# Optimization experiments

Measured on AMD Instinct MI355X. Metric: run time of the kernel, lower is better.

The kernel has to match this reference:

```python
import jax, jax.numpy as jnp
import numpy as np

N = 200000      # num nodes
E = 3200000     # num LBO edges (avg degree 16)
FIN = 64
FOUT = 64
K = 6           # Chebyshev order


def setup_inputs() -> dict:
    key = jax.random.key(0)
    k0, k1, k2, k3 = jax.random.split(key, 4)
    x = jax.random.normal(k0, (N, FIN), dtype=jnp.float32)
    LBO_index = jax.random.randint(k1, (2, E), 0, N)
    LBO_weight = jax.random.normal(k2, (E,), dtype=jnp.float32)
    stdv = float(np.sqrt(6.0 / (FIN + FOUT)))  # glorot uniform
    weight = jax.random.uniform(k3, (K, FIN, FOUT), dtype=jnp.float32,
                                minval=-stdv, maxval=stdv)
    bias = jnp.zeros((FOUT,), dtype=jnp.float32)
    return {"x": x, "LBO_index": LBO_index, "LBO_weight": LBO_weight,
            "weight": weight, "bias": bias}


def reference(x, LBO_index, LBO_weight, weight, bias):
    # __norm__: scale Laplacian weights by 2/(-lambda_max), lambda_max = 2.0 (sym)
    lambda_max = jnp.asarray(2.0, dtype=x.dtype)
    w = 2.0 * LBO_weight / (-lambda_max)
    w = jnp.where(w == jnp.inf, 0.0, w)
    # add self loops with fill value -1.0
    loops = jnp.arange(N)
    src = jnp.concatenate([LBO_index[0], loops])   # [E+N]
    dst = jnp.concatenate([LBO_index[1], loops])   # [E+N]
    norm = jnp.concatenate([w, jnp.full((N,), -1.0, dtype=w.dtype)])  # [E+N]

    def prop(z):
        # message = norm * z[src]; aggregate (sum) at dst
        msgs = norm[:, None] * z[src]                      # [E+N, F]
        return jax.ops.segment_sum(msgs, dst, num_segments=N)

    # Chebyshev recursion: T0 = x, T1 = L_hat x, Tk = 2 L_hat T_{k-1} - T_{k-2}
    Tx0 = x
    out = jnp.matmul(x, weight[0])
    Tx1 = prop(x)
    out = out + jnp.matmul(Tx1, weight[1])
    for k in range(2, K):
        Tx2 = 2.0 * prop(Tx1) - Tx0
        out = out + jnp.matmul(Tx2, weight[k])
        Tx0, Tx1 = Tx1, Tx2
    return out + bias
```

## Files before the change

kernel.cpp:

```cpp
#include <hip/hip_runtime.h>
#include <hip/hip_fp16.h>

#define FDIM 64
#define NB_SHIFT 10
#define NB_PAD 256
#define CH 4096


__global__ void hist_kernel(const int* __restrict__ dst, int* __restrict__ counts, int E) {
    int e = blockIdx.x * blockDim.x + threadIdx.x;
    if (e < E) atomicAdd(&counts[dst[e]], 1);
}

__global__ void scan_block_kernel(const int* __restrict__ in, int* __restrict__ out,
                                  int* __restrict__ blockSums, int n) {
    __shared__ int sdata[256];
    int t = threadIdx.x;
    int base = blockIdx.x * 1024 + t * 4;
    int v0 = (base + 0 < n) ? in[base + 0] : 0;
    int v1 = (base + 1 < n) ? in[base + 1] : 0;
    int v2 = (base + 2 < n) ? in[base + 2] : 0;
    int v3 = (base + 3 < n) ? in[base + 3] : 0;
    int tsum = v0 + v1 + v2 + v3;
    sdata[t] = tsum;
    __syncthreads();
    for (int off = 1; off < 256; off <<= 1) {
        int x = (t >= off) ? sdata[t - off] : 0;
        __syncthreads();
        sdata[t] += x;
        __syncthreads();
    }
    if (t == 255) blockSums[blockIdx.x] = sdata[255];
    int run = sdata[t] - tsum;
    if (base + 0 < n) out[base + 0] = run; run += v0;
    if (base + 1 < n) out[base + 1] = run; run += v1;
    if (base + 2 < n) out[base + 2] = run; run += v2;
    if (base + 3 < n) out[base + 3] = run;
}

__global__ void add_off_kernel(int* __restrict__ row_start, const int* __restrict__ blockSums,
                               int* __restrict__ bucket_cursor, int n) {
    int i = blockIdx.x * blockDim.x + threadIdx.x;
    if (i < n) {
        int v = row_start[i] + blockSums[i >> 10];
        row_start[i] = v;
        if ((i & ((1 << NB_SHIFT) - 1)) == 0) bucket_cursor[i >> NB_SHIFT] = v;
    }
}

__global__ __launch_bounds__(256) void bin_kernel(
        const int* __restrict__ src, const int* __restrict__ dst,
        const float* __restrict__ w, int* __restrict__ bucket_cursor,
        int2* __restrict__ binned_sv, unsigned short* __restrict__ binned_d,
        int E, int NB) {
    __shared__ int2 stage_sv[CH];
    __shared__ int  stage_d[CH];
    __shared__ int hist[NB_PAD], offs0[NB_PAD], run[NB_PAD], base[NB_PAD];

    int t = threadIdx.x;
    int c0 = blockIdx.x * CH;
    int valid = E - c0; if (valid > CH) valid = CH;

    for (int b = t; b < NB_PAD; b += 256) hist[b] = 0;
    __syncthreads();

    int  myd[16];
    int2 mysv[16];
    #pragma unroll
    for (int j = 0; j < 16; ++j) {
        int i = t + j * 256;
        if (i < valid) {
            int e = c0 + i;
            int d = dst[e];
            myd[j] = d;
            mysv[j] = make_int2(src[e], __float_as_int(-w[e]));
            atomicAdd(&hist[d >> NB_SHIFT], 1);
        } else myd[j] = -1;
    }
    __syncthreads();

    offs0[t] = hist[t];
    __syncthreads();
    for (int off = 1; off < 256; off <<= 1) {
        int x = (t >= off) ? offs0[t - off] : 0;
        __syncthreads();
        offs0[t] += x;
        __syncthreads();
    }
    int cnt_b = hist[t];
    int excl = offs0[t] - cnt_b;
    __syncthreads();
    offs0[t] = excl;
    run[t] = excl;
    base[t] = (t < NB && cnt_b > 0) ? atomicAdd(&bucket_cursor[t], cnt_b) : 0;
    __syncthreads();

    #pragma unroll
    for (int j = 0; j < 16; ++j) {
        if (myd[j] >= 0) {
            int b = myd[j] >> NB_SHIFT;
            int pos = atomicAdd(&run[b], 1);
            stage_sv[pos] = mysv[j];
            stage_d[pos]  = myd[j];
        }
    }
    __syncthreads();

    for (int i = t; i < valid; i += 256) {
        int d = stage_d[i];
        int b = d >> NB_SHIFT;
        int g = base[b] + (i - offs0[b]);
        binned_sv[g] = stage_sv[i];
        binned_d[g]  = (unsigned short)(d & ((1 << NB_SHIFT) - 1));
    }
}

__global__ __launch_bounds__(1024) void csr_kernel(
        const int* __restrict__ row_start, const int2* __restrict__ binned_sv,
        const unsigned short* __restrict__ binned_d,
        int2* __restrict__ colval, int E, int N) {
    __shared__ int lcur[1 << NB_SHIFT];
    int b = blockIdx.x;
    int t = threadIdx.x;
    int nbase = b << NB_SHIFT;
    int nextNode = (b + 1) << NB_SHIFT;

    int nloc = N - nbase; if (nloc > (1 << NB_SHIFT)) nloc = 1 << NB_SHIFT;
    if (t < nloc) lcur[t] = row_start[nbase + t];
    __syncthreads();

    int lo = row_start[nbase];
    int hi = (nextNode < N) ? row_start[nextNode] : E;
    for (int i = lo + t; i < hi; i += 1024) {
        int2 sv = binned_sv[i];
        int ld = binned_d[i];
        int p = atomicAdd(&lcur[ld], 1);
        colval[p] = sv;
    }
}


__global__ void convert_kernel(const float* __restrict__ x, __half* __restrict__ XH,
                               int total) {
    int i = (blockIdx.x * blockDim.x + threadIdx.x) * 4;
    if (i < total) {
        float4 v = *(const float4*)(x + i);
        __half2 h0 = __floats2half2_rn(v.x, v.y);
        __half2 h1 = __floats2half2_rn(v.z, v.w);
        int2 packed = make_int2(*(int*)&h0, *(int*)&h1);
        *(int2*)((char*)XH + (size_t)i * 2) = packed;
    }
}


#define GATHER_LOOP(SRC, ACC)                                                       \
    {                                                                               \
        int m = (cnt < 64) ? cnt : 64;                                              \
        int2 my = (lane < m) ? cv[lane] : make_int2(0, 0);                          \
        int cx = my.x;                                                              \
        float vv = __int_as_float(my.y);                                            \
        int j = 0;                                                                  \
        for (; j + 8 <= m; j += 8) {                                                \
            int c0 = __shfl(cx, j+0); float v0 = __shfl(vv, j+0);                   \
            int c1 = __shfl(cx, j+1); float v1 = __shfl(vv, j+1);                   \
            int c2 = __shfl(cx, j+2); float v2 = __shfl(vv, j+2);                   \
            int c3 = __shfl(cx, j+3); float v3 = __shfl(vv, j+3);                   \
            int c4 = __shfl(cx, j+4); float v4 = __shfl(vv, j+4);                   \
            int c5 = __shfl(cx, j+5); float v5 = __shfl(vv, j+5);                   \
            int c6 = __shfl(cx, j+6); float v6 = __shfl(vv, j+6);                   \
            int c7 = __shfl(cx, j+7); float v7 = __shfl(vv, j+7);                   \
            float t0 = __half2float(SRC[(size_t)c0 * FDIM + lane]);                 \
            float t1 = __half2float(SRC[(size_t)c1 * FDIM + lane]);                 \
            float t2 = __half2float(SRC[(size_t)c2 * FDIM + lane]);                 \
            float t3 = __half2float(SRC[(size_t)c3 * FDIM + lane]);                 \
            float t4 = __half2float(SRC[(size_t)c4 * FDIM + lane]);                 \
            float t5 = __half2float(SRC[(size_t)c5 * FDIM + lane]);                 \
            float t6 = __half2float(SRC[(size_t)c6 * FDIM + lane]);                 \
            float t7 = __half2float(SRC[(size_t)c7 * FDIM + lane]);                 \
            ACC += v0*t0 + v1*t1 + v2*t2 + v3*t3 + v4*t4 + v5*t5 + v6*t6 + v7*t7;   \
        }                                                                           \
        for (; j < m; ++j) {                                                        \
            int c = __shfl(cx, j); float v = __shfl(vv, j);                         \
            ACC += v * __half2float(SRC[(size_t)c * FDIM + lane]);                  \
        }                                                                           \
        for (int e2 = 64; e2 < cnt; ++e2) {                \
            int2 a = cv[e2];                                                        \
            ACC += __int_as_float(a.y) * __half2float(SRC[(size_t)a.x * FDIM + lane]); \
        }                                                                           \
    }

__global__ __launch_bounds__(256, 8) void pass1_kernel(
        const __half* __restrict__ XH, const int* __restrict__ row_start,
        const int* __restrict__ counts, const int2* __restrict__ colval,
        __half* __restrict__ T1H, int N) {
    int wid = threadIdx.x >> 6;
    int lane = threadIdx.x & 63;
    int node = blockIdx.x * 4 + wid;
    if (node >= N) return;

    float acc = -__half2float(XH[(size_t)node * FDIM + lane]);
    int s = row_start[node];
    int cnt = counts[node];
    const int2* cv = colval + s;
    GATHER_LOOP(XH, acc)
    T1H[(size_t)node * FDIM + lane] = __float2half(acc * 0.25f);
}

__global__ __launch_bounds__(256, 8) void passk_kernel(
        const __half* __restrict__ TcH, const __half* __restrict__ TpH,
        __half* __restrict__ TnH, const int* __restrict__ row_start,
        const int* __restrict__ counts, const int2* __restrict__ colval, int N) {
    int wid = threadIdx.x >> 6;
    int lane = threadIdx.x & 63;
    int node = blockIdx.x * 4 + wid;
    if (node >= N) return;

    size_t self = (size_t)node * FDIM + lane;
    int s = row_start[node];
    int cnt = counts[node];
    const int2* cv = colval + s;
    float acc = -__half2float(TcH[self]);
    GATHER_LOOP(TcH, acc)
    float tns = 0.5f * acc - 0.0625f * __half2float(TpH[self]);
    TnH[self] = __float2half(tns);
}


__global__ __launch_bounds__(256) void final_kernel(
        const __half* __restrict__ Tall, const float* __restrict__ W,
        const float* __restrict__ bias, float* __restrict__ out,
        int N, int K) {
    int wid = threadIdx.x >> 6;
    int lane = threadIdx.x & 63;
    int wg = blockIdx.x * 4 + wid;
    int node = (wg << 6) + lane;
    if (node >= N) return;
    size_t NT = (size_t)N * FDIM;

    float o[FDIM];
    #pragma unroll
    for (int l = 0; l < FDIM; ++l) o[l] = bias[l];

    float sig = 1.f;
    for (int k = 0; k < K; ++k) {
        const __half* Trow = Tall + (size_t)k * NT + (size_t)node * FDIM;
        const float* Wk = W + k * FDIM * FDIM;
        for (int i8 = 0; i8 < FDIM / 8; ++i8) {
            uint4 raw = *(const uint4*)(Trow + i8 * 8);
            const __half2* hp = (const __half2*)&raw;
            float tv[8];
            #pragma unroll
            for (int q = 0; q < 4; ++q) {
                float2 f = __half22float2(hp[q]);
                tv[2*q]   = sig * f.x;
                tv[2*q+1] = sig * f.y;
            }
            #pragma unroll
            for (int j = 0; j < 8; ++j) {
                const float* wrow = Wk + (i8 * 8 + j) * FDIM;
                #pragma unroll
                for (int l = 0; l < FDIM; ++l)
                    o[l] = fmaf(tv[j], wrow[l], o[l]);
            }
        }
        sig *= 4.f;
    }

    float* orow = out + (size_t)node * FDIM;
    #pragma unroll
    for (int l = 0; l < FDIM; l += 4)
        *(float4*)(orow + l) = make_float4(o[l], o[l+1], o[l+2], o[l+3]);
}


extern "C" void kernel_launch(void* const* d_in, const int* in_sizes, int n_in,
                              void* d_out, int out_size, void* d_ws, size_t ws_size,
                              hipStream_t stream) {
    const float* x      = (const float*)d_in[0];
    const int*   idx    = (const int*)d_in[1];
    const float* w      = (const float*)d_in[2];
    const float* weight = (const float*)d_in[3];
    const float* bias   = (const float*)d_in[4];
    float* out = (float*)d_out;

    const int N = in_sizes[0] / FDIM;
    const int E = in_sizes[2];
    const int K = in_sizes[3] / (FDIM * FDIM);
    const int NB = (N + (1 << NB_SHIFT) - 1) >> NB_SHIFT;

    const int* src = idx;
    const int* dst = idx + E;

    int* counts        = (int*)d_ws;
    int* row_start     = counts + N;
    int* blockSums     = row_start + N;
    int* bucket_cursor = blockSums + 512;
    int2* colval       = (int2*)(bucket_cursor + 256);
    __half* Tall       = (__half*)(colval + E);
    int2* binned_sv    = (int2*)Tall;
    unsigned short* binned_d = (unsigned short*)(Tall + (size_t)N * FDIM);

    hipMemsetAsync(counts, 0, (size_t)N * sizeof(int), stream);

    int eb = (E + 255) / 256;
    hist_kernel<<<eb, 256, 0, stream>>>(dst, counts, E);

    int nb = (N + 1023) / 1024;
    scan_block_kernel<<<nb, 256, 0, stream>>>(counts, row_start, blockSums, N);
    scan_block_kernel<<<1, 256, 0, stream>>>(blockSums, blockSums, blockSums + 500, nb);
    add_off_kernel<<<(N + 255) / 256, 256, 0, stream>>>(row_start, blockSums,
                                                        bucket_cursor, N);

    int bb = (E + CH - 1) / CH;
    bin_kernel<<<bb, 256, 0, stream>>>(src, dst, w, bucket_cursor,
                                       binned_sv, binned_d, E, NB);
    csr_kernel<<<NB, 1024, 0, stream>>>(row_start, binned_sv, binned_d,
                                        colval, E, N);

    convert_kernel<<<(N * FDIM + 1023) / 1024, 256, 0, stream>>>(x, Tall, N * FDIM);

    size_t NT = (size_t)N * FDIM;
    __half* T[8];
    for (int k = 0; k < K && k < 8; ++k) T[k] = Tall + (size_t)k * NT;

    int pb = (N + 3) / 4;
    pass1_kernel<<<pb, 256, 0, stream>>>(T[0], row_start, counts, colval, T[1], N);
    for (int k = 2; k < K; ++k) {
        passk_kernel<<<pb, 256, 0, stream>>>(T[k-1], T[k-2], T[k], row_start, counts,
                                             colval, N);
    }

    int fb = (((N + 63) >> 6) + 3) / 4;
    final_kernel<<<fb, 256, 0, stream>>>(Tall, weight, bias, out, N, K);
}
```

Measured before the change: 896.4 us.

## Replace scalar final projection with MFMA f16 matrix-core kernel

The final output projection, which summed K dense 64x64 matmuls with per-thread scalar FMAs over 64 accumulators, is replaced by an MFMA 16x16x32 f16 kernel. Each wavefront computes a 16-node tile. A new prep kernel transposes the weights, converts them to half precision, and folds in the power-of-4 scale factors. This moves the dense GEMM onto matrix cores and removes heavy register pressure, at the cost of fp16 weights, which could affect accuracy since the scale factors reach 4^5, and uncoalesced scalar output stores.

```diff
diff --git a/kernel.cpp b/kernel.cpp
--- a/kernel.cpp
+++ b/kernel.cpp
@@ -5,6 +5,9 @@
 #define NB_SHIFT 10
 #define NB_PAD 256
 #define CH 4096
+
+typedef __attribute__((ext_vector_type(8))) _Float16 half8;
+typedef __attribute__((ext_vector_type(4))) float floatx4;
 
 
 __global__ void hist_kernel(const int* __restrict__ dst, int* __restrict__ counts, int E) {
@@ -149,6 +152,20 @@
         __half2 h1 = __floats2half2_rn(v.z, v.w);
         int2 packed = make_int2(*(int*)&h0, *(int*)&h1);
         *(int2*)((char*)XH + (size_t)i * 2) = packed;
+    }
+}
+
+
+__global__ void prep_wt_kernel(const float* __restrict__ W, __half* __restrict__ WT,
+                               int K) {
+    int i = blockIdx.x * blockDim.x + threadIdx.x;
+    if (i < K * FDIM * FDIM) {
+        int tk  = i / (FDIM * FDIM);
+        int rem = i - tk * FDIM * FDIM;
+        int fin = rem >> 6;
+        int o   = rem & 63;
+        float sig = (float)(1 << (2 * tk));
+        WT[(size_t)o * (K * FDIM) + tk * FDIM + fin] = __float2half(sig * W[i]);
     }
 }
 
@@ -226,50 +243,51 @@
 }
 
 
-__global__ __launch_bounds__(256) void final_kernel(
-        const __half* __restrict__ Tall, const float* __restrict__ W,
+__global__ __launch_bounds__(256) void final_mfma_kernel(
+        const __half* __restrict__ Tall, const __half* __restrict__ WT,
         const float* __restrict__ bias, float* __restrict__ out,
         int N, int K) {
     int wid = threadIdx.x >> 6;
     int lane = threadIdx.x & 63;
-    int wg = blockIdx.x * 4 + wid;
-    int node = (wg << 6) + lane;
-    if (node >= N) return;
+    int tile = blockIdx.x * 4 + wid;
+    int nodeBase = tile << 4;
+    if (nodeBase >= N) return;
     size_t NT = (size_t)N * FDIM;
-
-    float o[FDIM];
+    int Kflat = K * FDIM;
+
+    int m = lane & 15;
+    int kgrp = lane >> 4;
+    int nodeA = nodeBase + m;
+    bool aok = nodeA < N;
+
+    floatx4 acc[4];
     #pragma unroll
-    for (int l = 0; l < FDIM; ++l) o[l] = bias[l];
-
-    float sig = 1.f;
-    for (int k = 0; k < K; ++k) {
-        const __half* Trow = Tall + (size_t)k * NT + (size_t)node * FDIM;
-        const float* Wk = W + k * FDIM * FDIM;
-        for (int i8 = 0; i8 < FDIM / 8; ++i8) {
-            uint4 raw = *(const uint4*)(Trow + i8 * 8);
-            const __half2* hp = (const __half2*)&raw;
-            float tv[8];
-            #pragma unroll
-            for (int q = 0; q < 4; ++q) {
-                float2 f = __half22float2(hp[q]);
-                tv[2*q]   = sig * f.x;
-                tv[2*q+1] = sig * f.y;
-            }
-            #pragma unroll
-            for (int j = 0; j < 8; ++j) {
-                const float* wrow = Wk + (i8 * 8 + j) * FDIM;
-                #pragma unroll
-                for (int l = 0; l < FDIM; ++l)
-                    o[l] = fmaf(tv[j], wrow[l], o[l]);
-            }
+    for (int f = 0; f < 4; ++f) {
+        float bv = bias[f * 16 + m];
+        acc[f] = (floatx4){bv, bv, bv, bv};
+    }
+
+    for (int kc = 0; kc < Kflat / 32; ++kc) {
+        int tk = kc >> 1;
+        int feat = ((kc & 1) << 5) + (kgrp << 3);
+        half8 a = aok ? *(const half8*)(Tall + (size_t)tk * NT + (size_t)nodeA * FDIM + feat)
+                      : (half8)(_Float16)0;
+        int kOff = (kc << 5) + (kgrp << 3);
+        #pragma unroll
+        for (int f = 0; f < 4; ++f) {
+            half8 b = *(const half8*)(WT + (size_t)(f * 16 + m) * Kflat + kOff);
+            acc[f] = __builtin_amdgcn_mfma_f32_16x16x32_f16(a, b, acc[f], 0, 0, 0);
         }
-        sig *= 4.f;
-    }
-
-    float* orow = out + (size_t)node * FDIM;
+    }
+
     #pragma unroll
-    for (int l = 0; l < FDIM; l += 4)
-        *(float4*)(orow + l) = make_float4(o[l], o[l+1], o[l+2], o[l+3]);
+    for (int f = 0; f < 4; ++f) {
+        #pragma unroll
+        for (int r = 0; r < 4; ++r) {
+            int nrow = nodeBase + (kgrp << 2) + r;
+            if (nrow < N) out[(size_t)nrow * FDIM + f * 16 + m] = acc[f][r];
+        }
+    }
 }
 
 
@@ -297,6 +315,7 @@
     int* bucket_cursor = blockSums + 512;
     int2* colval       = (int2*)(bucket_cursor + 256);
     __half* Tall       = (__half*)(colval + E);
+    __half* WT         = Tall + (size_t)K * N * FDIM;
     int2* binned_sv    = (int2*)Tall;
     unsigned short* binned_d = (unsigned short*)(Tall + (size_t)N * FDIM);
 
@@ -318,6 +337,7 @@
                                         colval, E, N);
 
     convert_kernel<<<(N * FDIM + 1023) / 1024, 256, 0, stream>>>(x, Tall, N * FDIM);
+    prep_wt_kernel<<<(K * FDIM * FDIM + 255) / 256, 256, 0, stream>>>(weight, WT, K);
 
     size_t NT = (size_t)N * FDIM;
     __half* T[8];
@@ -330,6 +350,6 @@
                                              colval, N);
     }
 
-    int fb = (((N + 63) >> 6) + 3) / 4;
-    final_kernel<<<fb, 256, 0, stream>>>(Tall, weight, bias, out, N, K);
-}
+    int tiles = (N + 15) >> 4;
+    final_mfma_kernel<<<(tiles + 3) / 4, 256, 0, stream>>>(Tall, WT, bias, out, N, K);
+}
```

Result: faster. 841.6 us (-6.1%).
